# Kernel tuning notes

Measured on AMD Instinct MI355X. Metric: run time of the kernel, lower is better.

Reference implementation:

```python
import jax, jax.numpy as jnp
import numpy as np

N_LEVELS = 16
N_FEAT = 2
LOG2_HASHMAP = 19
HASHMAP_SIZE = 1 << LOG2_HASHMAP
BASE_RES = 16.0
FINEST_RES = 512.0
B_POINTS = 524288


def ngp_hash(coords, log2_size):
    # instant-NGP spatial hash: xor of coord * prime, masked to table size.
    # uint32 arithmetic wraps exactly like torch int32 for the masked low bits.
    primes = jnp.array([1, 2654435761, 805459861], dtype=jnp.uint32)
    c = coords.astype(jnp.uint32) * primes  # (..., 3)
    h = c[..., 0] ^ c[..., 1] ^ c[..., 2]
    return (h & jnp.uint32((1 << log2_size) - 1)).astype(jnp.int32)


def setup_inputs() -> dict:
    key = jax.random.key(0)
    k1, k2 = jax.random.split(key)
    # points strictly inside the unit bounding box
    x = jax.random.uniform(k1, (B_POINTS, 3), jnp.float32) * 0.998 + 0.001
    # embedding table init U(-1e-4, 1e-4), matching init_debug_vector
    table = (jax.random.uniform(k2, (HASHMAP_SIZE * N_LEVELS, N_FEAT), jnp.float32) * 2.0 - 1.0) * 1e-4
    box_min = jnp.zeros((3,), jnp.float32)
    box_max = jnp.ones((3,), jnp.float32)
    return {"x": x, "table": table, "box_min": box_min, "box_max": box_max}


def reference(x, table, box_min, box_max):
    B = x.shape[0]
    # per-level growth factor b and resolutions (L,1,1)
    b = jnp.exp((jnp.log(FINEST_RES) - jnp.log(BASE_RES)) / (N_LEVELS - 1))
    resolution = jnp.floor(BASE_RES * b ** jnp.arange(N_LEVELS, dtype=jnp.float32))[:, None, None]
    bmin = box_min[None, None]  # (1,1,3)
    bmax = box_max[None, None]
    grid_size = (bmax - bmin) / resolution  # (L,1,3)

    xl = x[None]  # (1,B,3)
    bottom_left = ((xl - bmin) / grid_size).astype(jnp.int32)  # (L,B,3)
    voxel_min = bottom_left.astype(x.dtype) * grid_size + bmin  # (L,B,3)
    voxel_max = voxel_min + grid_size

    # 8 corner offsets, i-major order as in the torch box_offsets
    offsets = jnp.array([[i, j, k] for i in (0, 1) for j in (0, 1) for k in (0, 1)], dtype=jnp.int32)  # (8,3)
    corners = bottom_left[:, :, None, :] + offsets[None, None]  # (L,B,8,3)

    level_off = (jnp.arange(N_LEVELS, dtype=jnp.int32) * HASHMAP_SIZE)[:, None, None]
    idx = ngp_hash(corners, LOG2_HASHMAP) + level_off  # (L,B,8)
    ve = table[idx]  # (L,B,8,F) hash-gather

    w = (xl - voxel_min) / (voxel_max - voxel_min)  # (L,B,3)
    wx, wy, wz = w[..., 0:1], w[..., 1:2], w[..., 2:3]
    c00 = ve[:, :, 0] * (1 - wx) + ve[:, :, 4] * wx
    c01 = ve[:, :, 1] * (1 - wx) + ve[:, :, 5] * wx
    c10 = ve[:, :, 2] * (1 - wx) + ve[:, :, 6] * wx
    c11 = ve[:, :, 3] * (1 - wx) + ve[:, :, 7] * wx
    c0 = c00 * (1 - wy) + c10 * wy
    c1 = c01 * (1 - wy) + c11 * wy
    c = c0 * (1 - wz) + c1 * wz  # (L,B,F)

    # permute(1,2,0) then flatten last two dims -> (B, F*L)
    return jnp.transpose(c, (1, 2, 0)).reshape(B, N_FEAT * N_LEVELS)
```

## Files before the change

kernel.cpp:

```cpp
#include <hip/hip_runtime.h>
#include <cstdint>


constexpr int NLEV = 16;
constexpr uint32_t HM_MASK = (1u << 19) - 1;

__device__ __constant__ double c_res[NLEV] = {
    16.0, 20.0, 25.0, 32.0, 40.0, 50.0, 64.0, 80.0,
    101.0, 128.0, 161.0, 203.0, 256.0, 322.0, 406.0, 512.0
};

__device__ __forceinline__ void ngp_eval_point(
    int b, int lev,
    const float* __restrict__ x,
    const float2* __restrict__ tab2,
    float bm0, float bm1, float bm2,
    float d0, float d1, float d2,
    float& f0, float& f1)
{
    const float fx0 = x[3 * b + 0];
    const float fx1 = x[3 * b + 1];
    const float fx2 = x[3 * b + 2];

    const double res = c_res[lev];
    const double g0 = (double)d0 / res;
    const double g1 = (double)d1 / res;
    const double g2 = (double)d2 / res;
    const double q0 = (double)(fx0 - bm0) / g0;
    const double q1 = (double)(fx1 - bm1) / g1;
    const double q2 = (double)(fx2 - bm2) / g2;
    const int i0 = (int)q0;
    const int i1 = (int)q1;
    const int i2 = (int)q2;
    const float w0 = (float)(q0 - (double)i0);
    const float w1 = (float)(q1 - (double)i1);
    const float w2 = (float)(q2 - (double)i2);

    const uint32_t P1 = 2654435761u, P2 = 805459861u;
    const uint32_t h0a = (uint32_t)i0;
    const uint32_t h0b = h0a + 1u;
    const uint32_t h1a = (uint32_t)i1 * P1;
    const uint32_t h1b = h1a + P1;
    const uint32_t h2a = (uint32_t)i2 * P2;
    const uint32_t h2b = h2a + P2;
    const uint32_t base = (uint32_t)lev << 19;

    const float2 v000 = tab2[base + ((h0a ^ h1a ^ h2a) & HM_MASK)];
    const float2 v001 = tab2[base + ((h0a ^ h1a ^ h2b) & HM_MASK)];
    const float2 v010 = tab2[base + ((h0a ^ h1b ^ h2a) & HM_MASK)];
    const float2 v011 = tab2[base + ((h0a ^ h1b ^ h2b) & HM_MASK)];
    const float2 v100 = tab2[base + ((h0b ^ h1a ^ h2a) & HM_MASK)];
    const float2 v101 = tab2[base + ((h0b ^ h1a ^ h2b) & HM_MASK)];
    const float2 v110 = tab2[base + ((h0b ^ h1b ^ h2a) & HM_MASK)];
    const float2 v111 = tab2[base + ((h0b ^ h1b ^ h2b) & HM_MASK)];

    const float u0 = 1.0f - w0, u1 = 1.0f - w1, u2 = 1.0f - w2;
    const float waa = u1 * u2;
    const float wab = u1 * w2;
    const float wba = w1 * u2;
    const float wbb = w1 * w2;

    f0 = u0 * (waa * v000.x + wab * v001.x + wba * v010.x + wbb * v011.x)
       + w0 * (waa * v100.x + wab * v101.x + wba * v110.x + wbb * v111.x);
    f1 = u0 * (waa * v000.y + wab * v001.y + wba * v010.y + wbb * v011.y)
       + w0 * (waa * v100.y + wab * v101.y + wba * v110.y + wbb * v111.y);
}

__global__ __launch_bounds__(256)
void ngp_levels_kernel(const float* __restrict__ x,
                       const float* __restrict__ table,
                       const float* __restrict__ box_min,
                       const float* __restrict__ box_max,
                       float2* __restrict__ ws,
                       int B, int chunks)
{
    const int xcd = blockIdx.x & 7;
    const int s   = blockIdx.x >> 3;
    const int lev   = (s < chunks) ? xcd : (15 - xcd);
    const int chunk = (s < chunks) ? s : (s - chunks);
    const int b = chunk * 256 + threadIdx.x;
    if (b >= B) return;

    const float bm0 = box_min[0], bm1 = box_min[1], bm2 = box_min[2];
    const float d0 = box_max[0] - bm0;
    const float d1 = box_max[1] - bm1;
    const float d2 = box_max[2] - bm2;

    float f0, f1;
    ngp_eval_point(b, lev, x, (const float2*)table,
                   bm0, bm1, bm2, d0, d1, d2, f0, f1);

    ws[(size_t)lev * B + b] = make_float2(f0, f1);
}

constexpr int LDS_STRIDE = 257;

__global__ __launch_bounds__(256)
void ngp_transpose_kernel(const float2* __restrict__ ws,
                          float* __restrict__ out,
                          int B)
{
    __shared__ float lds[32 * LDS_STRIDE];

    const int t  = threadIdx.x;
    const int P0 = blockIdx.x * 256;

#pragma unroll
    for (int l = 0; l < NLEV; ++l) {
        const float2 v = ws[(size_t)l * B + P0 + t];
        lds[(2 * l)     * LDS_STRIDE + t] = v.x;
        lds[(2 * l + 1) * LDS_STRIDE + t] = v.y;
    }
    __syncthreads();

    const int p_lo = t >> 3;
    const int f    = (t >> 2) & 1;
    const int l0   = (t & 3) * 4;
#pragma unroll
    for (int j = 0; j < 8; ++j) {
        const int p = j * 32 + p_lo;
        float4 v;
        v.x = lds[(2 * (l0 + 0) + f) * LDS_STRIDE + p];
        v.y = lds[(2 * (l0 + 1) + f) * LDS_STRIDE + p];
        v.z = lds[(2 * (l0 + 2) + f) * LDS_STRIDE + p];
        v.w = lds[(2 * (l0 + 3) + f) * LDS_STRIDE + p];
        *(float4*)(out + (size_t)P0 * 32 + j * 1024 + t * 4) = v;
    }
}

__global__ __launch_bounds__(256)
void ngp_embed_fused_kernel(const float* __restrict__ x,
                            const float* __restrict__ table,
                            const float* __restrict__ box_min,
                            const float* __restrict__ box_max,
                            float* __restrict__ out,
                            int B)
{
    const int gid = blockIdx.x * 256 + threadIdx.x;
    const int b = gid >> 4;
    const int l = gid & 15;
    if (b >= B) return;

    const float bm0 = box_min[0], bm1 = box_min[1], bm2 = box_min[2];
    const float d0 = box_max[0] - bm0;
    const float d1 = box_max[1] - bm1;
    const float d2 = box_max[2] - bm2;

    float f0, f1;
    ngp_eval_point(b, l, x, (const float2*)table,
                   bm0, bm1, bm2, d0, d1, d2, f0, f1);

    out[b * 32 + l]      = f0;
    out[b * 32 + 16 + l] = f1;
}

extern "C" void kernel_launch(void* const* d_in, const int* in_sizes, int n_in,
                              void* d_out, int out_size, void* d_ws, size_t ws_size,
                              hipStream_t stream) {
    const float* x       = (const float*)d_in[0];
    const float* table   = (const float*)d_in[1];
    const float* box_min = (const float*)d_in[2];
    const float* box_max = (const float*)d_in[3];
    float* out = (float*)d_out;

    const int B = in_sizes[0] / 3;
    const size_t ws_needed = (size_t)B * NLEV * sizeof(float2);

    if (ws_size >= ws_needed && (B % 256) == 0) {
        const int chunks = B / 256;
        const int gridA = 8 * 2 * chunks;
        hipLaunchKernelGGL(ngp_levels_kernel, dim3(gridA), dim3(256), 0, stream,
                           x, table, box_min, box_max, (float2*)d_ws, B, chunks);
        const int gridB = B / 256;
        hipLaunchKernelGGL(ngp_transpose_kernel, dim3(gridB), dim3(256), 0, stream,
                           (const float2*)d_ws, out, B);
    } else {
        const int total = B * NLEV;
        const int blocks = (total + 255) / 256;
        hipLaunchKernelGGL(ngp_embed_fused_kernel, dim3(blocks), dim3(256), 0, stream,
                           x, table, box_min, box_max, out, B);
    }
}
```

Measured before the change: 336.0 us.

## Pair x-adjacent corner gathers into float4 loads via even/odd point compaction

```diff
diff --git a/kernel.cpp b/kernel.cpp
--- a/kernel.cpp
+++ b/kernel.cpp
@@ -10,14 +10,31 @@
     101.0, 128.0, 161.0, 203.0, 256.0, 322.0, 406.0, 512.0
 };
 
-__device__ __forceinline__ void ngp_eval_point(
-    int b, int lev,
-    const float* __restrict__ x,
-    const float2* __restrict__ tab2,
-    float bm0, float bm1, float bm2,
-    float d0, float d1, float d2,
-    float& f0, float& f1)
+__global__ __launch_bounds__(256)
+void ngp_levels_kernel(const float* __restrict__ x,
+                       const float* __restrict__ table,
+                       const float* __restrict__ box_min,
+                       const float* __restrict__ box_max,
+                       float2* __restrict__ ws,
+                       int B, int chunks)
 {
+    __shared__ int s_cnt[4];
+    __shared__ uint32_t s_h0[256], s_h1[256], s_h2[256];
+    __shared__ float s_w0[256], s_w1[256], s_w2[256];
+    __shared__ float s_f0[256], s_f1[256];
+
+    const int xcd = blockIdx.x & 7;
+    const int s   = blockIdx.x >> 3;
+    const int lev   = (s < chunks) ? xcd : (15 - xcd);
+    const int chunk = (s < chunks) ? s : (s - chunks);
+    const int t = threadIdx.x;
+    const int b = chunk * 256 + t;
+
+    const float bm0 = box_min[0], bm1 = box_min[1], bm2 = box_min[2];
+    const float d0 = box_max[0] - bm0;
+    const float d1 = box_max[1] - bm1;
+    const float d2 = box_max[2] - bm2;
+
     const float fx0 = x[3 * b + 0];
     const float fx1 = x[3 * b + 1];
     const float fx2 = x[3 * b + 2];
@@ -37,60 +54,90 @@
     const float w2 = (float)(q2 - (double)i2);
 
     const uint32_t P1 = 2654435761u, P2 = 805459861u;
-    const uint32_t h0a = (uint32_t)i0;
-    const uint32_t h0b = h0a + 1u;
-    const uint32_t h1a = (uint32_t)i1 * P1;
-    const uint32_t h1b = h1a + P1;
-    const uint32_t h2a = (uint32_t)i2 * P2;
-    const uint32_t h2b = h2a + P2;
-    const uint32_t base = (uint32_t)lev << 19;
-
-    const float2 v000 = tab2[base + ((h0a ^ h1a ^ h2a) & HM_MASK)];
-    const float2 v001 = tab2[base + ((h0a ^ h1a ^ h2b) & HM_MASK)];
-    const float2 v010 = tab2[base + ((h0a ^ h1b ^ h2a) & HM_MASK)];
-    const float2 v011 = tab2[base + ((h0a ^ h1b ^ h2b) & HM_MASK)];
-    const float2 v100 = tab2[base + ((h0b ^ h1a ^ h2a) & HM_MASK)];
-    const float2 v101 = tab2[base + ((h0b ^ h1a ^ h2b) & HM_MASK)];
-    const float2 v110 = tab2[base + ((h0b ^ h1b ^ h2a) & HM_MASK)];
-    const float2 v111 = tab2[base + ((h0b ^ h1b ^ h2b) & HM_MASK)];
-
-    const float u0 = 1.0f - w0, u1 = 1.0f - w1, u2 = 1.0f - w2;
-    const float waa = u1 * u2;
-    const float wab = u1 * w2;
-    const float wba = w1 * u2;
-    const float wbb = w1 * w2;
-
-    f0 = u0 * (waa * v000.x + wab * v001.x + wba * v010.x + wbb * v011.x)
-       + w0 * (waa * v100.x + wab * v101.x + wba * v110.x + wbb * v111.x);
-    f1 = u0 * (waa * v000.y + wab * v001.y + wba * v010.y + wbb * v011.y)
-       + w0 * (waa * v100.y + wab * v101.y + wba * v110.y + wbb * v111.y);
-}
-
-__global__ __launch_bounds__(256)
-void ngp_levels_kernel(const float* __restrict__ x,
-                       const float* __restrict__ table,
-                       const float* __restrict__ box_min,
-                       const float* __restrict__ box_max,
-                       float2* __restrict__ ws,
-                       int B, int chunks)
-{
-    const int xcd = blockIdx.x & 7;
-    const int s   = blockIdx.x >> 3;
-    const int lev   = (s < chunks) ? xcd : (15 - xcd);
-    const int chunk = (s < chunks) ? s : (s - chunks);
-    const int b = chunk * 256 + threadIdx.x;
-    if (b >= B) return;
-
-    const float bm0 = box_min[0], bm1 = box_min[1], bm2 = box_min[2];
-    const float d0 = box_max[0] - bm0;
-    const float d1 = box_max[1] - bm1;
-    const float d2 = box_max[2] - bm2;
-
-    float f0, f1;
-    ngp_eval_point(b, lev, x, (const float2*)table,
-                   bm0, bm1, bm2, d0, d1, d2, f0, f1);
-
-    ws[(size_t)lev * B + b] = make_float2(f0, f1);
+    const uint32_t h0 = (uint32_t)i0;
+    const uint32_t h1 = (uint32_t)i1 * P1;
+    const uint32_t h2 = (uint32_t)i2 * P2;
+
+    const int lane = t & 63;
+    const int wv   = t >> 6;
+    const bool evn = ((h0 & 1u) == 0u);
+    const unsigned long long bal = __ballot(evn);
+    const unsigned long long below = (lane == 63)
+        ? (bal & ~(1ull << 63)) : (bal & ((1ull << (lane + 1)) - 1) >> 1);
+    const unsigned long long mlow = (1ull << lane) - 1ull;
+    const int lowerE = __popcll(bal & mlow);
+    const int waveE  = __popcll(bal);
+    (void)below;
+    if (lane == 0) s_cnt[wv] = waveE;
+    __syncthreads();
+
+    int evenBase = 0, totalEven = 0;
+#pragma unroll
+    for (int i = 0; i < 4; ++i) {
+        const int c = s_cnt[i];
+        if (i < wv) evenBase += c;
+        totalEven += c;
+    }
+    const int oddBase = totalEven + (wv * 64 - evenBase);
+    const int slot = evn ? (evenBase + lowerE) : (oddBase + (lane - lowerE));
+
+    s_h0[slot] = h0;  s_h1[slot] = h1;  s_h2[slot] = h2;
+    s_w0[slot] = w0;  s_w1[slot] = w1;  s_w2[slot] = w2;
+    __syncthreads();
+
+    {
+        const uint32_t H0 = s_h0[t];
+        const uint32_t H1a = s_h1[t], H1b = H1a + P1;
+        const uint32_t H2a = s_h2[t], H2b = H2a + P2;
+        const float W0 = s_w0[t], W1 = s_w1[t], W2 = s_w2[t];
+        const float U0 = 1.0f - W0, U1 = 1.0f - W1, U2 = 1.0f - W2;
+        const float waa = U1 * U2;
+        const float wab = U1 * W2;
+        const float wba = W1 * U2;
+        const float wbb = W1 * W2;
+        const uint32_t base = (uint32_t)lev << 19;
+        const float2* __restrict__ tab2 = (const float2*)table;
+
+        float acc0, acc1;
+        if (t < totalEven) {
+            const float4* __restrict__ tab4 = (const float4*)table;
+            acc0 = 0.0f; acc1 = 0.0f;
+#define NGP_PAIR(HJK, WYZ)                                                    \
+            {                                                                 \
+                const uint32_t idx = (H0 ^ (HJK)) & HM_MASK;                  \
+                const float4 q = tab4[(base + idx) >> 1];                     \
+                const float wlo = (idx & 1u) ? W0 : U0;                       \
+                const float whi = (idx & 1u) ? U0 : W0;                       \
+                acc0 += (WYZ) * (wlo * q.x + whi * q.z);                      \
+                acc1 += (WYZ) * (wlo * q.y + whi * q.w);                      \
+            }
+            NGP_PAIR(H1a ^ H2a, waa)
+            NGP_PAIR(H1a ^ H2b, wab)
+            NGP_PAIR(H1b ^ H2a, wba)
+            NGP_PAIR(H1b ^ H2b, wbb)
+#undef NGP_PAIR
+        } else {
+            const uint32_t H0b = H0 + 1u;
+            const float2 v000 = tab2[base + ((H0  ^ H1a ^ H2a) & HM_MASK)];
+            const float2 v001 = tab2[base + ((H0  ^ H1a ^ H2b) & HM_MASK)];
+            const float2 v010 = tab2[base + ((H0  ^ H1b ^ H2a) & HM_MASK)];
+            const float2 v011 = tab2[base + ((H0  ^ H1b ^ H2b) & HM_MASK)];
+            const float2 v100 = tab2[base + ((H0b ^ H1a ^ H2a) & HM_MASK)];
+            const float2 v101 = tab2[base + ((H0b ^ H1a ^ H2b) & HM_MASK)];
+            const float2 v110 = tab2[base + ((H0b ^ H1b ^ H2a) & HM_MASK)];
+            const float2 v111 = tab2[base + ((H0b ^ H1b ^ H2b) & HM_MASK)];
+
+            acc0 = U0 * (waa * v000.x + wab * v001.x + wba * v010.x + wbb * v011.x)
+                 + W0 * (waa * v100.x + wab * v101.x + wba * v110.x + wbb * v111.x);
+            acc1 = U0 * (waa * v000.y + wab * v001.y + wba * v010.y + wbb * v011.y)
+                 + W0 * (waa * v100.y + wab * v101.y + wba * v110.y + wbb * v111.y);
+        }
+        s_f0[t] = acc0;
+        s_f1[t] = acc1;
+    }
+    __syncthreads();
+
+    ws[(size_t)lev * B + b] = make_float2(s_f0[slot], s_f1[slot]);
 }
 
 constexpr int LDS_STRIDE = 257;
@@ -146,9 +193,50 @@
     const float d1 = box_max[1] - bm1;
     const float d2 = box_max[2] - bm2;
 
-    float f0, f1;
-    ngp_eval_point(b, l, x, (const float2*)table,
-                   bm0, bm1, bm2, d0, d1, d2, f0, f1);
+    const float fx0 = x[3 * b + 0];
+    const float fx1 = x[3 * b + 1];
+    const float fx2 = x[3 * b + 2];
+
+    const double res = c_res[l];
+    const double q0 = (double)(fx0 - bm0) / ((double)d0 / res);
+    const double q1 = (double)(fx1 - bm1) / ((double)d1 / res);
+    const double q2 = (double)(fx2 - bm2) / ((double)d2 / res);
+    const int i0 = (int)q0;
+    const int i1 = (int)q1;
+    const int i2 = (int)q2;
+    const float w0 = (float)(q0 - (double)i0);
+    const float w1 = (float)(q1 - (double)i1);
+    const float w2 = (float)(q2 - (double)i2);
+
+    const uint32_t P1 = 2654435761u, P2 = 805459861u;
+    const uint32_t h0a = (uint32_t)i0;
+    const uint32_t h0b = h0a + 1u;
+    const uint32_t h1a = (uint32_t)i1 * P1;
+    const uint32_t h1b = h1a + P1;
+    const uint32_t h2a = (uint32_t)i2 * P2;
+    const uint32_t h2b = h2a + P2;
+    const uint32_t base = (uint32_t)l << 19;
+    const float2* __restrict__ tab2 = (const float2*)table;
+
+    const float2 v000 = tab2[base + ((h0a ^ h1a ^ h2a) & HM_MASK)];
+    const float2 v001 = tab2[base + ((h0a ^ h1a ^ h2b) & HM_MASK)];
+    const float2 v010 = tab2[base + ((h0a ^ h1b ^ h2a) & HM_MASK)];
+    const float2 v011 = tab2[base + ((h0a ^ h1b ^ h2b) & HM_MASK)];
+    const float2 v100 = tab2[base + ((h0b ^ h1a ^ h2a) & HM_MASK)];
+    const float2 v101 = tab2[base + ((h0b ^ h1a ^ h2b) & HM_MASK)];
+    const float2 v110 = tab2[base + ((h0b ^ h1b ^ h2a) & HM_MASK)];
+    const float2 v111 = tab2[base + ((h0b ^ h1b ^ h2b) & HM_MASK)];
+
+    const float u0 = 1.0f - w0, u1 = 1.0f - w1, u2 = 1.0f - w2;
+    const float waa = u1 * u2;
+    const float wab = u1 * w2;
+    const float wba = w1 * u2;
+    const float wbb = w1 * w2;
+
+    const float f0 = u0 * (waa * v000.x + wab * v001.x + wba * v010.x + wbb * v011.x)
+                   + w0 * (waa * v100.x + wab * v101.x + wba * v110.x + wbb * v111.x);
+    const float f1 = u0 * (waa * v000.y + wab * v001.y + wba * v010.y + wbb * v011.y)
+                   + w0 * (waa * v100.y + wab * v101.y + wba * v110.y + wbb * v111.y);
 
     out[b * 32 + l]      = f0;
     out[b * 32 + 16 + l] = f1;
```

New measurement: 320.8 us. 4.5% less time.
